# Optimization experiments

Measured on AMD Instinct MI355X. Metric: run time of the kernel, lower is better.

Reference implementation:

```python
import jax, jax.numpy as jnp
import numpy as np

E = 1024   # embed_dim
H = 16     # num_heads
D = E // H # head dim = 64
NUM_BUCKETS = 32
MAX_DISTANCE = 128


def _relative_position_bucket(rel, num_buckets=NUM_BUCKETS, max_distance=MAX_DISTANCE):
    # T5-style bucketing (bidirectional): sign half + log-spaced far buckets.
    nb = num_buckets // 2
    buckets = (rel > 0).astype(jnp.int32) * nb
    rel = jnp.abs(rel)
    max_exact = nb // 2
    is_small = rel < max_exact
    # clamp to >=1 before log to avoid -inf on the masked-out branch
    rel_f = jnp.maximum(rel, 1).astype(jnp.float32)
    large = max_exact + (
        jnp.log(rel_f / max_exact) / np.log(max_distance / max_exact) * (nb - max_exact)
    ).astype(jnp.int32)
    large = jnp.minimum(large, nb - 1)
    return buckets + jnp.where(is_small, rel, large)


def setup_inputs() -> dict:
    key = jax.random.key(0)
    ks = jax.random.split(key, 6)
    B, S, K = 2, 2048, 2048
    w = 0.02
    return {
        "hidden_states": jax.random.normal(ks[0], (B, S, E), jnp.float32),
        "key_value_states": jax.random.normal(ks[1], (B, K, E), jnp.float32),
        "Wq": jax.random.normal(ks[2], (E, E), jnp.float32) * w,
        "Wkv": jax.random.normal(ks[3], (E, 2 * E), jnp.float32) * w,
        "Wo": jax.random.normal(ks[4], (E, E), jnp.float32) * w,
        "rel_bias": jax.random.normal(ks[5], (NUM_BUCKETS, H), jnp.float32) * w,
    }


def reference(hidden_states, key_value_states, Wq, Wkv, Wo, rel_bias):
    B, S, _ = hidden_states.shape
    K = key_value_states.shape[1]
    # projections (no bias, no 1/sqrt(d) scaling — T5 style)
    q = (hidden_states @ Wq).reshape(B, S, H, D).transpose(0, 2, 1, 3)      # [B,H,S,D]
    kv = (key_value_states @ Wkv).reshape(B, K, 2, H, D)
    k = kv[:, :, 0].transpose(0, 2, 1, 3)                                   # [B,H,K,D]
    v = kv[:, :, 1].transpose(0, 2, 1, 3)                                   # [B,H,K,D]
    scores = jnp.einsum('bhsd,bhkd->bhsk', q, k)                            # [B,H,S,K]
    # relative position bias
    rel = jnp.arange(K)[None, :] - jnp.arange(S)[:, None]                   # [S,K]
    buckets = _relative_position_bucket(rel)                                # [S,K]
    bias = rel_bias[buckets].transpose(2, 0, 1)[None]                       # [1,H,S,K]
    scores = scores + bias
    attn = jax.nn.softmax(scores.astype(jnp.float32), axis=-1).astype(scores.dtype)
    out = jnp.einsum('bhsk,bhkd->bshd', attn, v).reshape(B, S, E)
    return out @ Wo
```

## Files before the change

kernel.cpp:

```cpp
#include <hip/hip_runtime.h>
#include <hip/hip_bf16.h>
#include <math.h>

typedef __hip_bfloat16 bf16;
typedef __bf16 bf16x4 __attribute__((ext_vector_type(4)));
typedef __bf16 bf16x8 __attribute__((ext_vector_type(8)));
typedef float f32x4 __attribute__((ext_vector_type(4)));
typedef float f32x16 __attribute__((ext_vector_type(16)));
typedef unsigned short us4 __attribute__((ext_vector_type(4)));

#define LOG2E 1.44269504088896340736f

#if defined(__has_builtin)
#if __has_builtin(__builtin_amdgcn_exp2f)
#define EXP2(x) __builtin_amdgcn_exp2f(x)
#else
#define EXP2(x) exp2f(x)
#endif
#else
#define EXP2(x) exp2f(x)
#endif

__device__ inline __bf16 f2b(float f) {
  __hip_bfloat16 h = __float2bfloat16(f);
  return *reinterpret_cast<__bf16*>(&h);
}
__device__ inline unsigned short b2u(float f) {
  __hip_bfloat16 h = __float2bfloat16(f);
  return *reinterpret_cast<unsigned short*>(&h);
}
__device__ inline unsigned short b2u_fast(float f) {
  union { float f; unsigned u; } v;
  v.f = f;
  return (unsigned short)((v.u + 0x8000u) >> 16);
}
__device__ inline bf16x8 ld16(const bf16* p) {
  bf16x4 lo = *(const bf16x4*)p;
  bf16x4 hi = *(const bf16x4*)(p + 4);
  return __builtin_shufflevector(lo, hi, 0, 1, 2, 3, 4, 5, 6, 7);
}
__device__ inline void st16(bf16* p, uint4 v) {
  *(uint2*)p = make_uint2(v.x, v.y);
  *(uint2*)(p + 4) = make_uint2(v.z, v.w);
}
__device__ inline us4 shfl32_us4(us4 v) {
  uint2 u = *(uint2*)&v;
  u.x = __shfl_xor(u.x, 32);
  u.y = __shfl_xor(u.y, 32);
  return *(us4*)&u;
}
__device__ inline bf16x8 mk8(us4 lo, us4 hi) {
  bf16x4 l = *(bf16x4*)&lo;
  bf16x4 h = *(bf16x4*)&hi;
  return __builtin_shufflevector(l, h, 0, 1, 2, 3, 4, 5, 6, 7);
}
__device__ inline void async16(const bf16* g, bf16* l) {
  __builtin_amdgcn_global_load_lds(
      (const __attribute__((address_space(1))) unsigned int*)g,
      (__attribute__((address_space(3))) unsigned int*)l, 16, 0, 0);
}

__global__ void cast2_k(const float* __restrict__ a, const float* __restrict__ b,
                        bf16* __restrict__ oa, bf16* __restrict__ ob) {
  int gid = blockIdx.x * 256 + threadIdx.x;
  const float* in = (gid < 524288) ? a : b;
  bf16* out = (gid < 524288) ? oa : ob;
  int i = (gid & 524287) * 8;
  float4 a0 = *(const float4*)(in + i);
  float4 a1 = *(const float4*)(in + i + 4);
  bf16x8 v;
  v[0] = f2b(a0.x); v[1] = f2b(a0.y); v[2] = f2b(a0.z); v[3] = f2b(a0.w);
  v[4] = f2b(a1.x); v[5] = f2b(a1.y); v[6] = f2b(a1.z); v[7] = f2b(a1.w);
  *(bf16x8*)(out + i) = v;
}

__global__ void transpose_all_k(const float* __restrict__ Wq, const float* __restrict__ Wkv,
                                const float* __restrict__ Wo, bf16* __restrict__ WqT,
                                bf16* __restrict__ WkvT, bf16* __restrict__ WoT) {
  __shared__ float tile[32][33];
  int z = blockIdx.z;
  const float* in = z == 0 ? Wq : (z == 1 ? Wkv : Wo);
  bf16* out = z == 0 ? WqT : (z == 1 ? WkvT : WoT);
  int cols = z == 1 ? 2048 : 1024;
  int c0 = blockIdx.x * 32;
  if (c0 >= cols) return;
  int r0 = blockIdx.y * 32;
  int tx = threadIdx.x, ty = threadIdx.y;
  for (int i = ty; i < 32; i += 8)
    tile[i][tx] = in[(size_t)(r0 + i) * cols + c0 + tx];
  __syncthreads();
  for (int i = ty; i < 32; i += 8)
    out[(size_t)(c0 + i) * 1024 + r0 + tx] = __float2bfloat16(tile[tx][i]);
}

__global__ void bias_lut_k(const float* __restrict__ rel_bias, float* __restrict__ lut) {
  int r = blockIdx.x * blockDim.x + threadIdx.x;
  if (r >= 4096) return;
  int rel = r - 2048;
  int b = rel > 0 ? 16 : 0;
  int ar = rel < 0 ? -rel : rel;
  int idx;
  if (ar < 8) {
    idx = b + ar;
  } else {
    double t = log((double)ar / 8.0) / log(16.0) * 8.0;
    int lg = 8 + (int)t;
    if (lg > 15) lg = 15;
    idx = b + lg;
  }
  for (int h = 0; h < 16; ++h)
    lut[h * 4096 + r] = rel_bias[idx * 16 + h] * LOG2E;
}

__global__ __launch_bounds__(256) void gemm_qkv_k(const bf16* __restrict__ hbf,
                                                  const bf16* __restrict__ kbf,
                                                  const bf16* __restrict__ WqT,
                                                  const bf16* __restrict__ WkvT,
                                                  bf16* __restrict__ Qb,
                                                  bf16* __restrict__ Kb,
                                                  bf16* __restrict__ Vt) {
  __shared__ __align__(16) bf16 As[128 * 32];
  __shared__ __align__(16) bf16 Bs[128 * 32];
  const int tid = threadIdx.x;
  const int lane = tid & 63;
  const int w = tid >> 6;
  const int wm = (w >> 1) * 64;
  const int wn = (w & 1) * 64;
  const int l15 = lane & 15;
  const int quad = lane >> 4;
  const int srow = lane >> 2;
  const int skg = lane & 3;

  const bool isQ = blockIdx.y < 8;
  const bf16* A = isQ ? hbf : kbf;
  const bf16* Bt = isQ ? WqT : WkvT;
  const int n0 = (isQ ? blockIdx.y : blockIdx.y - 8) * 128;
  const int m0 = blockIdx.x * 128;
  const bool isV = (!isQ) && (n0 >= 1024);

  f32x4 acc[4][4];
#pragma unroll
  for (int i = 0; i < 4; ++i)
#pragma unroll
    for (int j = 0; j < 4; ++j) acc[i][j] = (f32x4){0.f, 0.f, 0.f, 0.f};

  for (int k0 = 0; k0 < 1024; k0 += 32) {
    __syncthreads();
#pragma unroll
    for (int rep = 0; rep < 2; ++rep) {
      int seg = w * 2 + rep;
      async16(A + (size_t)(m0 + seg * 16 + srow) * 1024 + k0 + skg * 8, As + seg * 512);
      async16(Bt + (size_t)(n0 + seg * 16 + srow) * 1024 + k0 + skg * 8, Bs + seg * 512);
    }
    __syncthreads();
    bf16x8 af[4], bfr[4];
#pragma unroll
    for (int i = 0; i < 4; ++i)
      af[i] = *(const bf16x8*)(As + (wm + i * 16 + l15) * 32 + quad * 8);
#pragma unroll
    for (int j = 0; j < 4; ++j)
      bfr[j] = *(const bf16x8*)(Bs + (wn + j * 16 + l15) * 32 + quad * 8);
    if (isV) {
#pragma unroll
      for (int i = 0; i < 4; ++i)
#pragma unroll
        for (int j = 0; j < 4; ++j)
          acc[i][j] = __builtin_amdgcn_mfma_f32_16x16x32_bf16(af[i], bfr[j], acc[i][j], 0, 0, 0);
    } else {
#pragma unroll
      for (int i = 0; i < 4; ++i)
#pragma unroll
        for (int j = 0; j < 4; ++j)
          acc[i][j] = __builtin_amdgcn_mfma_f32_16x16x32_bf16(bfr[j], af[i], acc[i][j], 0, 0, 0);
    }
  }

  if (isV) {
#pragma unroll
    for (int i = 0; i < 4; ++i) {
      int gmb = m0 + wm + i * 16 + quad * 4;
      int b = gmb >> 11, kp = gmb & 2047;
#pragma unroll
      for (int j = 0; j < 4; ++j) {
        int gn = n0 + wn + j * 16 + l15;
        int h = (gn >> 6) & 15, d = gn & 63;
        us4 pk;
#pragma unroll
        for (int r = 0; r < 4; ++r) pk[r] = b2u(acc[i][j][r]);
        *(us4*)(Vt + ((((size_t)b * 16 + h) * 64 + d) << 11) + kp) = pk;
      }
    }
    return;
  }
  const float scale = isQ ? LOG2E : 1.0f;
  bf16* dst = isQ ? Qb : Kb;
#pragma unroll
  for (int i = 0; i < 4; ++i) {
    int gm = m0 + wm + i * 16 + l15;
    int b = gm >> 11, s = gm & 2047;
#pragma unroll
    for (int j = 0; j < 4; ++j) {
      int gn = n0 + wn + j * 16 + quad * 4;
      int h = (gn >> 6) & 15, d0 = gn & 63;
      us4 pk;
#pragma unroll
      for (int r = 0; r < 4; ++r) pk[r] = b2u(acc[i][j][r] * scale);
      *(us4*)(dst + ((((size_t)b * 16 + h) * 2048 + s) << 6) + d0) = pk;
    }
  }
}

__global__ __launch_bounds__(256) void gemm_o_k(const bf16* __restrict__ A,
                                                const bf16* __restrict__ Bt,
                                                float* __restrict__ C0) {
  __shared__ __align__(16) bf16 As[128 * 32];
  __shared__ __align__(16) bf16 Bs[64 * 32];
  const int tid = threadIdx.x;
  const int lane = tid & 63;
  const int w = tid >> 6;
  const int wm = w * 32;
  const int m0 = blockIdx.x * 128;
  const int n0 = blockIdx.y * 64;
  const int l15 = lane & 15;
  const int quad = lane >> 4;
  const int srow = lane >> 2;
  const int skg = lane & 3;

  f32x4 acc[2][4];
#pragma unroll
  for (int i = 0; i < 2; ++i)
#pragma unroll
    for (int j = 0; j < 4; ++j) acc[i][j] = (f32x4){0.f, 0.f, 0.f, 0.f};

  for (int k0 = 0; k0 < 1024; k0 += 32) {
    __syncthreads();
#pragma unroll
    for (int rep = 0; rep < 2; ++rep) {
      int seg = w * 2 + rep;
      async16(A + (size_t)(m0 + seg * 16 + srow) * 1024 + k0 + skg * 8, As + seg * 512);
    }
    async16(Bt + (size_t)(n0 + w * 16 + srow) * 1024 + k0 + skg * 8, Bs + w * 512);
    __syncthreads();
    bf16x8 af[2], bfr[4];
#pragma unroll
    for (int i = 0; i < 2; ++i)
      af[i] = *(const bf16x8*)(As + (wm + i * 16 + l15) * 32 + quad * 8);
#pragma unroll
    for (int j = 0; j < 4; ++j)
      bfr[j] = *(const bf16x8*)(Bs + (j * 16 + l15) * 32 + quad * 8);
#pragma unroll
    for (int i = 0; i < 2; ++i)
#pragma unroll
      for (int j = 0; j < 4; ++j)
        acc[i][j] = __builtin_amdgcn_mfma_f32_16x16x32_bf16(bfr[j], af[i], acc[i][j], 0, 0, 0);
  }
#pragma unroll
  for (int i = 0; i < 2; ++i) {
    int gm = m0 + wm + i * 16 + l15;
#pragma unroll
    for (int j = 0; j < 4; ++j) {
      int gn = n0 + j * 16 + quad * 4;
      *(f32x4*)(C0 + (size_t)gm * 1024 + gn) = acc[i][j];
    }
  }
}

#define STK 68
#define SVK 136
__global__ __launch_bounds__(256) void attn_k(const bf16* __restrict__ Qb,
                                              const bf16* __restrict__ Kb,
                                              const bf16* __restrict__ Vt,
                                              const float* __restrict__ lut,
                                              bf16* __restrict__ Ob) {
  __shared__ float lbias[2176];
  __shared__ __align__(16) bf16 Ks[128 * STK];
  __shared__ __align__(16) bf16 Vs[64 * SVK];

  const int tid = threadIdx.x;
  const int lane = tid & 63;
  const int w = tid >> 6;
  const int q31 = lane & 31;
  const int half = lane >> 5;

  const int qt = blockIdx.x;
  const int bh = blockIdx.y;
  const int h = bh & 15, b = bh >> 4;
  const int qb = qt * 128;

  const int gbase = h * 4096 + 1921 - qb;
  for (int t = tid; t < 2175; t += 256) lbias[t] = lut[gbase + t];

  const size_t base = (size_t)bh * 2048 * 64;
  const size_t vbase = (size_t)bh * 64 * 2048;
  const int qg = qb + w * 32 + q31;

  bf16x8 qf[4];
#pragma unroll
  for (int c = 0; c < 4; ++c)
    qf[c] = *(const bf16x8*)(Qb + base + (size_t)qg * 64 + c * 16 + half * 8);

  f32x16 oacc[2];
#pragma unroll
  for (int dj = 0; dj < 2; ++dj)
#pragma unroll
    for (int r = 0; r < 16; ++r) oacc[dj][r] = 0.f;
  float m_run = -INFINITY, l_run = 0.f;

  uint4 kreg[4], vreg[4];
#pragma unroll
  for (int rep = 0; rep < 4; ++rep) {
    int slot = tid + rep * 256;
    kreg[rep] = *(const uint4*)(Kb + base + (size_t)(slot >> 3) * 64 + (slot & 7) * 8);
    vreg[rep] = *(const uint4*)(Vt + vbase + (size_t)(slot >> 4) * 2048 + (slot & 15) * 8);
  }

  for (int kt = 0; kt < 2048; kt += 128) {
    __syncthreads();
#pragma unroll
    for (int rep = 0; rep < 4; ++rep) {
      int slot = tid + rep * 256;
      st16(Ks + (slot >> 3) * STK + (slot & 7) * 8, kreg[rep]);
      st16(Vs + (slot >> 4) * SVK + (slot & 15) * 8, vreg[rep]);
    }
    __syncthreads();
    if (kt + 128 < 2048) {
#pragma unroll
      for (int rep = 0; rep < 4; ++rep) {
        int slot = tid + rep * 256;
        kreg[rep] = *(const uint4*)(Kb + base + (size_t)(kt + 128 + (slot >> 3)) * 64 + (slot & 7) * 8);
        vreg[rep] = *(const uint4*)(Vt + vbase + (size_t)(slot >> 4) * 2048 + kt + 128 + (slot & 15) * 8);
      }
    }

    f32x16 sacc[4];
#pragma unroll
    for (int mt = 0; mt < 4; ++mt) {
#pragma unroll
      for (int r = 0; r < 16; ++r) sacc[mt][r] = 0.f;
#pragma unroll
      for (int c = 0; c < 4; ++c) {
        bf16x8 kf = ld16(Ks + (mt * 32 + q31) * STK + c * 16 + half * 8);
        sacc[mt] = __builtin_amdgcn_mfma_f32_32x32x16_bf16(kf, qf[c], sacc[mt], 0, 0, 0);
      }
    }

    const int xbase = kt + 127 + 4 * half - w * 32 - q31;
    float mx = -INFINITY;
#pragma unroll
    for (int mt = 0; mt < 4; ++mt)
#pragma unroll
      for (int g = 0; g < 4; ++g) {
        int x0 = xbase + mt * 32 + 8 * g;
#pragma unroll
        for (int rr = 0; rr < 4; ++rr) {
          float s = sacc[mt][4 * g + rr] + lbias[x0 + rr];
          sacc[mt][4 * g + rr] = s;
          mx = fmaxf(mx, s);
        }
      }
    mx = fmaxf(mx, __shfl_xor(mx, 32));
    float mnew = fmaxf(m_run, mx);
    float alpha = EXP2(m_run - mnew);
    m_run = mnew;
    float sum = 0.f;
#pragma unroll
    for (int mt = 0; mt < 4; ++mt)
#pragma unroll
      for (int r = 0; r < 16; ++r) {
        float p = EXP2(sacc[mt][r] - mnew);
        sacc[mt][r] = p;
        sum += p;
      }
    sum += __shfl_xor(sum, 32);
    l_run = l_run * alpha + sum;

    us4 ownq[4][4], rcv[4][2];
#pragma unroll
    for (int mt = 0; mt < 4; ++mt) {
#pragma unroll
      for (int a = 0; a < 4; ++a) {
        us4 pk;
#pragma unroll
        for (int bb = 0; bb < 4; ++bb) pk[bb] = b2u_fast(sacc[mt][4 * a + bb]);
        ownq[mt][a] = pk;
      }
      us4 s0 = half ? ownq[mt][0] : ownq[mt][1];
      us4 s1 = half ? ownq[mt][2] : ownq[mt][3];
      rcv[mt][0] = shfl32_us4(s0);
      rcv[mt][1] = shfl32_us4(s1);
    }

#pragma unroll
    for (int dj = 0; dj < 2; ++dj)
#pragma unroll
      for (int r = 0; r < 16; ++r) oacc[dj][r] *= alpha;

#pragma unroll
    for (int c = 0; c < 8; ++c) {
      int mt = c >> 1, p = c & 1;
      bf16x8 pfc = half ? mk8(rcv[mt][p], ownq[mt][2 * p + 1])
                        : mk8(ownq[mt][2 * p], rcv[mt][p]);
#pragma unroll
      for (int dj = 0; dj < 2; ++dj) {
        bf16x8 vf = ld16(Vs + (dj * 32 + q31) * SVK + c * 16 + half * 8);
        oacc[dj] = __builtin_amdgcn_mfma_f32_32x32x16_bf16(vf, pfc, oacc[dj], 0, 0, 0);
      }
    }
  }

  float inv = 1.0f / l_run;
#pragma unroll
  for (int dj = 0; dj < 2; ++dj)
#pragma unroll
    for (int g = 0; g < 4; ++g) {
      us4 pk;
#pragma unroll
      for (int rr = 0; rr < 4; ++rr) pk[rr] = b2u(oacc[dj][4 * g + rr] * inv);
      int d0 = dj * 32 + 8 * g + 4 * half;
      *(us4*)(Ob + ((size_t)(b * 2048 + qg)) * 1024 + h * 64 + d0) = pk;
    }
}

extern "C" void kernel_launch(void* const* d_in, const int* in_sizes, int n_in,
                              void* d_out, int out_size, void* d_ws, size_t ws_size,
                              hipStream_t stream) {
  const float* hidden = (const float*)d_in[0];
  const float* kvs    = (const float*)d_in[1];
  const float* Wq     = (const float*)d_in[2];
  const float* Wkv    = (const float*)d_in[3];
  const float* Wo     = (const float*)d_in[4];
  const float* relb   = (const float*)d_in[5];
  float* out = (float*)d_out;

  char* ws = (char*)d_ws;
  bf16* WqT  = (bf16*)(ws + (size_t)0);
  bf16* WkvT = (bf16*)(ws + ((size_t)2 << 20));
  bf16* WoT  = (bf16*)(ws + ((size_t)6 << 20));
  bf16* Ob   = (bf16*)(ws + ((size_t)8 << 20));
  bf16* hbf  = Ob;
  bf16* Qb   = (bf16*)(ws + ((size_t)16 << 20));
  bf16* Kb   = (bf16*)(ws + ((size_t)24 << 20));
  bf16* Vt   = (bf16*)(ws + ((size_t)32 << 20));
  float* LUT = (float*)(ws + ((size_t)40 << 20));
  bf16* kbf  = (bf16*)d_out;

  transpose_all_k<<<dim3(64, 32, 3), dim3(32, 8), 0, stream>>>(Wq, Wkv, Wo, WqT, WkvT, WoT);
  bias_lut_k<<<16, 256, 0, stream>>>(relb, LUT);
  cast2_k<<<4096, 256, 0, stream>>>(hidden, kvs, hbf, kbf);

  gemm_qkv_k<<<dim3(32, 24), 256, 0, stream>>>(hbf, kbf, WqT, WkvT, Qb, Kb, Vt);
  attn_k<<<dim3(16, 32), 256, 0, stream>>>(Qb, Kb, Vt, LUT, Ob);
  gemm_o_k<<<dim3(32, 16), 256, 0, stream>>>(Ob, WoT, out);
}
```

Baseline: 233.2 us.

## Split attention key range across two warp groups per block and merge softmax states

The attention kernel now launches 512 threads per block: two groups of four waves each process alternating 128-key tiles of the same 128 queries, each with its own shared-memory K/V buffers. At the end, the second group writes its running max, sum and output accumulator to shared memory, and the first group merges the two partial softmax states before writing output. It also folds the relative bias into the MFMA accumulator initialisation and uses tree reductions for max and sum. The aim is to double the waves available for latency hiding with only 512 blocks, at the cost of more shared memory, register pressure under launch bounds (512,4), and an extra merge step.

```diff
diff --git a/kernel.cpp b/kernel.cpp
--- a/kernel.cpp
+++ b/kernel.cpp
@@ -267,20 +267,29 @@
 
 #define STK 68
 #define SVK 136
-__global__ __launch_bounds__(256) void attn_k(const bf16* __restrict__ Qb,
-                                              const bf16* __restrict__ Kb,
-                                              const bf16* __restrict__ Vt,
-                                              const float* __restrict__ lut,
-                                              bf16* __restrict__ Ob) {
-  __shared__ float lbias[2176];
-  __shared__ __align__(16) bf16 Ks[128 * STK];
-  __shared__ __align__(16) bf16 Vs[64 * SVK];
+#define KS_OFF 8704
+#define VS_OFF 43520
+__global__ __launch_bounds__(512, 4) void attn_k(const bf16* __restrict__ Qb,
+                                                 const bf16* __restrict__ Kb,
+                                                 const bf16* __restrict__ Vt,
+                                                 const float* __restrict__ lut,
+                                                 bf16* __restrict__ Ob) {
+  __shared__ __align__(16) char smem[78336];
+  float* lbias = (float*)smem;
+  bf16* Ksb = (bf16*)(smem + KS_OFF);
+  bf16* Vsb = (bf16*)(smem + VS_OFF);
 
   const int tid = threadIdx.x;
   const int lane = tid & 63;
   const int w = tid >> 6;
+  const int wq = w & 3;
+  const int kg = w >> 2;
+  const int t256 = tid & 255;
   const int q31 = lane & 31;
   const int half = lane >> 5;
+
+  bf16* Ks = Ksb + kg * (128 * STK);
+  bf16* Vs = Vsb + kg * (64 * SVK);
 
   const int qt = blockIdx.x;
   const int bh = blockIdx.y;
@@ -288,11 +297,11 @@
   const int qb = qt * 128;
 
   const int gbase = h * 4096 + 1921 - qb;
-  for (int t = tid; t < 2175; t += 256) lbias[t] = lut[gbase + t];
+  for (int t = tid; t < 2175; t += 512) lbias[t] = lut[gbase + t];
 
   const size_t base = (size_t)bh * 2048 * 64;
   const size_t vbase = (size_t)bh * 64 * 2048;
-  const int qg = qb + w * 32 + q31;
+  const int qg = qb + wq * 32 + q31;
 
   bf16x8 qf[4];
 #pragma unroll
@@ -306,37 +315,45 @@
     for (int r = 0; r < 16; ++r) oacc[dj][r] = 0.f;
   float m_run = -INFINITY, l_run = 0.f;
 
+  const int kt0 = kg * 128;
+
   uint4 kreg[4], vreg[4];
 #pragma unroll
   for (int rep = 0; rep < 4; ++rep) {
-    int slot = tid + rep * 256;
-    kreg[rep] = *(const uint4*)(Kb + base + (size_t)(slot >> 3) * 64 + (slot & 7) * 8);
-    vreg[rep] = *(const uint4*)(Vt + vbase + (size_t)(slot >> 4) * 2048 + (slot & 15) * 8);
-  }
-
-  for (int kt = 0; kt < 2048; kt += 128) {
+    int slot = t256 + rep * 256;
+    kreg[rep] = *(const uint4*)(Kb + base + (size_t)(kt0 + (slot >> 3)) * 64 + (slot & 7) * 8);
+    vreg[rep] = *(const uint4*)(Vt + vbase + (size_t)(slot >> 4) * 2048 + kt0 + (slot & 15) * 8);
+  }
+
+  for (int it = 0; it < 8; ++it) {
+    const int kt = it * 256 + kt0;
     __syncthreads();
 #pragma unroll
     for (int rep = 0; rep < 4; ++rep) {
-      int slot = tid + rep * 256;
+      int slot = t256 + rep * 256;
       st16(Ks + (slot >> 3) * STK + (slot & 7) * 8, kreg[rep]);
       st16(Vs + (slot >> 4) * SVK + (slot & 15) * 8, vreg[rep]);
     }
     __syncthreads();
-    if (kt + 128 < 2048) {
+    if (it < 7) {
+      const int nkt = kt + 256;
 #pragma unroll
       for (int rep = 0; rep < 4; ++rep) {
-        int slot = tid + rep * 256;
-        kreg[rep] = *(const uint4*)(Kb + base + (size_t)(kt + 128 + (slot >> 3)) * 64 + (slot & 7) * 8);
-        vreg[rep] = *(const uint4*)(Vt + vbase + (size_t)(slot >> 4) * 2048 + kt + 128 + (slot & 15) * 8);
+        int slot = t256 + rep * 256;
+        kreg[rep] = *(const uint4*)(Kb + base + (size_t)(nkt + (slot >> 3)) * 64 + (slot & 7) * 8);
+        vreg[rep] = *(const uint4*)(Vt + vbase + (size_t)(slot >> 4) * 2048 + nkt + (slot & 15) * 8);
       }
     }
 
+    const int xbase = kt + 127 + 4 * half - wq * 32 - q31;
     f32x16 sacc[4];
 #pragma unroll
     for (int mt = 0; mt < 4; ++mt) {
 #pragma unroll
-      for (int r = 0; r < 16; ++r) sacc[mt][r] = 0.f;
+      for (int a2 = 0; a2 < 4; ++a2)
+#pragma unroll
+        for (int rr = 0; rr < 4; ++rr)
+          sacc[mt][4 * a2 + rr] = lbias[xbase + mt * 32 + 8 * a2 + rr];
 #pragma unroll
       for (int c = 0; c < 4; ++c) {
         bf16x8 kf = ld16(Ks + (mt * 32 + q31) * STK + c * 16 + half * 8);
@@ -344,33 +361,33 @@
       }
     }
 
-    const int xbase = kt + 127 + 4 * half - w * 32 - q31;
-    float mx = -INFINITY;
-#pragma unroll
-    for (int mt = 0; mt < 4; ++mt)
-#pragma unroll
-      for (int g = 0; g < 4; ++g) {
-        int x0 = xbase + mt * 32 + 8 * g;
-#pragma unroll
-        for (int rr = 0; rr < 4; ++rr) {
-          float s = sacc[mt][4 * g + rr] + lbias[x0 + rr];
-          sacc[mt][4 * g + rr] = s;
-          mx = fmaxf(mx, s);
-        }
-      }
+    float mxa[4];
+#pragma unroll
+    for (int mt = 0; mt < 4; ++mt) {
+      float p[8];
+#pragma unroll
+      for (int i = 0; i < 8; ++i) p[i] = fmaxf(sacc[mt][2 * i], sacc[mt][2 * i + 1]);
+#pragma unroll
+      for (int i = 0; i < 4; ++i) p[i] = fmaxf(p[i], p[i + 4]);
+      mxa[mt] = fmaxf(fmaxf(p[0], p[1]), fmaxf(p[2], p[3]));
+    }
+    float mx = fmaxf(fmaxf(mxa[0], mxa[1]), fmaxf(mxa[2], mxa[3]));
     mx = fmaxf(mx, __shfl_xor(mx, 32));
     float mnew = fmaxf(m_run, mx);
     float alpha = EXP2(m_run - mnew);
     m_run = mnew;
-    float sum = 0.f;
+    f32x4 sv = (f32x4){0.f, 0.f, 0.f, 0.f};
 #pragma unroll
     for (int mt = 0; mt < 4; ++mt)
 #pragma unroll
-      for (int r = 0; r < 16; ++r) {
-        float p = EXP2(sacc[mt][r] - mnew);
-        sacc[mt][r] = p;
-        sum += p;
-      }
+      for (int a2 = 0; a2 < 4; ++a2)
+#pragma unroll
+        for (int rr = 0; rr < 4; ++rr) {
+          float p = EXP2(sacc[mt][4 * a2 + rr] - mnew);
+          sacc[mt][4 * a2 + rr] = p;
+          sv[rr] += p;
+        }
+    float sum = (sv[0] + sv[1]) + (sv[2] + sv[3]);
     sum += __shfl_xor(sum, 32);
     l_run = l_run * alpha + sum;
 
@@ -408,14 +425,36 @@
     }
   }
 
-  float inv = 1.0f / l_run;
+  __syncthreads();
+  float* mbuf = (float*)smem;
+  if (kg) {
+    float* p = mbuf + ((size_t)(wq * 64 + lane)) * 35;
+    p[0] = m_run;
+    p[1] = l_run;
+#pragma unroll
+    for (int dj = 0; dj < 2; ++dj)
+#pragma unroll
+      for (int r = 0; r < 16; ++r) p[2 + dj * 16 + r] = oacc[dj][r];
+  }
+  __syncthreads();
+  if (kg) return;
+
+  const float* p = mbuf + ((size_t)(wq * 64 + lane)) * 35;
+  float m1 = p[0], l1 = p[1];
+  float mf = fmaxf(m_run, m1);
+  float a0 = EXP2(m_run - mf);
+  float a1 = EXP2(m1 - mf);
+  float inv = 1.0f / (l_run * a0 + l1 * a1);
+  float w0 = a0 * inv, w1 = a1 * inv;
+
 #pragma unroll
   for (int dj = 0; dj < 2; ++dj)
 #pragma unroll
     for (int g = 0; g < 4; ++g) {
       us4 pk;
 #pragma unroll
-      for (int rr = 0; rr < 4; ++rr) pk[rr] = b2u(oacc[dj][4 * g + rr] * inv);
+      for (int rr = 0; rr < 4; ++rr)
+        pk[rr] = b2u(oacc[dj][4 * g + rr] * w0 + p[2 + dj * 16 + 4 * g + rr] * w1);
       int d0 = dj * 32 + 8 * g + 4 * half;
       *(us4*)(Ob + ((size_t)(b * 2048 + qg)) * 1024 + h * 64 + d0) = pk;
     }
@@ -449,6 +488,6 @@
   cast2_k<<<4096, 256, 0, stream>>>(hidden, kvs, hbf, kbf);
 
   gemm_qkv_k<<<dim3(32, 24), 256, 0, stream>>>(hbf, kbf, WqT, WkvT, Qb, Kb, Vt);
-  attn_k<<<dim3(16, 32), 256, 0, stream>>>(Qb, Kb, Vt, LUT, Ob);
+  attn_k<<<dim3(16, 32), 512, 0, stream>>>(Qb, Kb, Vt, LUT, Ob);
   gemm_o_k<<<dim3(32, 16), 256, 0, stream>>>(Ob, WoT, out);
 }
```

New measurement: 340.3 us. +45.9%, slower.
